# Kernel optimization log

Hardware: AMD Instinct MI355X
Metric: run time of the kernel (lower is better)

Reference implementation:

```python
import jax, jax.numpy as jnp
import numpy as np

V, H, B, S, J, T, NOP = 30000, 512, 16, 256, 10, 8, 4
NEG = -1e9


def setup_inputs() -> dict:
    key = jax.random.key(0)
    ks = jax.random.split(key, 10)
    return {
        "x": jax.random.randint(ks[0], (B, S), 0, V),
        "encoder_output": jax.random.normal(ks[1], (B, S, H), jnp.float32),
        "encoder_hidden": jax.random.normal(ks[2], (B, H), jnp.float32),
        "max_len": T,
        "emb_W": jax.random.normal(ks[3], (V, H), jnp.float32) * 0.02,
        "slot_emb": jax.random.normal(ks[4], (J, H), jnp.float32) * 0.1,
        "W_ih": jax.random.normal(ks[5], (3 * H, H), jnp.float32) * 0.02,
        "W_hh": jax.random.normal(ks[6], (3 * H, H), jnp.float32) * 0.02,
        "b_ih": jnp.zeros((3 * H,), jnp.float32),
        "b_hh": jnp.zeros((3 * H,), jnp.float32),
        "w_gen_W": jax.random.normal(ks[7], (1, 3 * H), jnp.float32) * 0.02,
        "w_gen_b": jnp.zeros((1,), jnp.float32),
        "action_W": jax.random.normal(ks[8], (NOP, H), jnp.float32) * 0.02,
        "action_b": jnp.zeros((NOP,), jnp.float32),
    }


def gru_step(xin, h, W_ih, W_hh, b_ih, b_hh):
    # xin, h: (J, B, H). PyTorch GRU gate order: r, z, n.
    gi = xin @ W_ih.T + b_ih
    gh = h @ W_hh.T + b_hh
    ir, iz, inn = jnp.split(gi, 3, axis=-1)
    hr, hz, hn = jnp.split(gh, 3, axis=-1)
    r = jax.nn.sigmoid(ir + hr)
    z = jax.nn.sigmoid(iz + hz)
    n = jnp.tanh(inn + r * hn)
    return (1.0 - z) * n + z * h


def reference(x, encoder_output, encoder_hidden, max_len, emb_W, slot_emb,
              W_ih, W_hh, b_ih, b_hh, w_gen_W, w_gen_b, action_W, action_b):
    nJ, nH = slot_emb.shape
    nB, nS = x.shape
    nV = emb_W.shape[0]
    mask = (x == 0)  # (B, S) pad mask
    xJ = jnp.broadcast_to(x[None], (nJ, nB, nS))
    jidx = jnp.arange(nJ)[:, None, None]
    bidx = jnp.arange(nB)[None, :, None]

    w0 = jnp.broadcast_to(slot_emb[:, None, :], (nJ, nB, nH))  # slot query per slot
    h0 = jnp.broadcast_to(encoder_hidden[None], (nJ, nB, nH))

    def step(carry, _):
        w, h = carry
        h = gru_step(w, h, W_ih, W_hh, b_ih, b_hh)
        # attention over encoder states
        attn_e = jnp.einsum('bsh,jbh->jbs', encoder_output, h)
        attn_e = jnp.where(mask[None], NEG, attn_e)
        attn_hist = jax.nn.softmax(attn_e, axis=-1)          # (J,B,S)
        context = jnp.einsum('jbs,bsh->jbh', attn_hist, encoder_output)
        # vocab distribution
        attn_vocab = jax.nn.softmax(h @ emb_W.T, axis=-1)    # (J,B,V)
        # pointer-generator mix
        gen_in = jnp.concatenate([w, h, context], axis=-1)   # (J,B,3H)
        p_gen = jax.nn.sigmoid(gen_in @ w_gen_W.T + w_gen_b) # (J,B,1)
        p_ctx = jnp.zeros((nJ, nB, nV), attn_vocab.dtype).at[jidx, bidx, xJ].add(attn_hist)
        p_final = p_gen * attn_vocab + (1.0 - p_gen) * p_ctx # (J,B,V)
        w_idx = jnp.argmax(p_final, axis=-1)                 # greedy next token
        w_next = emb_W[w_idx]                                # (J,B,H)
        return (w_next, h), (p_final, context)

    (_, _), (p_all, ctx_all) = jax.lax.scan(step, (w0, h0), None, length=max_len)
    # gate head uses context from first decode step (k == 0)
    gates = ctx_all[0] @ action_W.T + action_b               # (J,B,n_op)
    all_gate = jnp.transpose(gates, (1, 0, 2))               # (B,J,n_op)
    all_point = jnp.transpose(p_all, (2, 1, 0, 3))           # (B,J,T,V)
    return all_gate, all_point
```

## Files before the change

### kernel.cpp

```cpp
#include <hip/hip_runtime.h>
#include <math.h>

#define V 30000
#define H 512
#define NB 16
#define NS 256
#define NJ 10
#define NT 8
#define NOPS 4
#define NR 160
#define EV 30720
#define NEGV -1e9f

typedef __attribute__((ext_vector_type(8))) short short8;
typedef __attribute__((ext_vector_type(4))) short short4v;
typedef __attribute__((ext_vector_type(4))) float f32x4;

__device__ inline float bf2f(unsigned short s) {
    union { unsigned int u; float f; } c; c.u = ((unsigned int)s) << 16;
    return c.f;
}
__device__ inline unsigned short f2bf(float f) {
    union { float f; unsigned int u; } c; c.f = f;
    unsigned int u = c.u;
    u += 0x7fffu + ((u >> 16) & 1u);
    return (unsigned short)(u >> 16);
}
__device__ inline unsigned long long packkey(float f, int v) {
    union { float f; unsigned int u; } c; c.f = f;
    return ((unsigned long long)c.u << 32) | (unsigned int)(0x7FFFFFFF - v);
}

__global__ void k_setup_emb(const float* __restrict__ emb, unsigned short* __restrict__ emb_bf, int n8) {
    int gid = blockIdx.x * 256 + threadIdx.x;
    if (gid >= n8) return;
    const float4* src = (const float4*)emb + (size_t)gid * 2;
    float4 a = src[0], b = src[1];
    short8 o;
    o[0] = (short)f2bf(a.x); o[1] = (short)f2bf(a.y); o[2] = (short)f2bf(a.z); o[3] = (short)f2bf(a.w);
    o[4] = (short)f2bf(b.x); o[5] = (short)f2bf(b.y); o[6] = (short)f2bf(b.z); o[7] = (short)f2bf(b.w);
    *(short8*)(emb_bf + (size_t)gid * 8) = o;
}

__global__ void k_setup_small(const float* __restrict__ Wih, const float* __restrict__ Whh,
    unsigned short* wih_hi, unsigned short* wih_lo, unsigned short* whh_hi, unsigned short* whh_lo,
    const float* __restrict__ slot, const float* __restrict__ ench,
    float* w_g, unsigned short* w_hi, unsigned short* w_lo,
    float* h_g, unsigned short* h_hi, unsigned short* h_lo)
{
    int gid = blockIdx.x * 256 + threadIdx.x;
    if (gid < 786432) {
        float v1 = Wih[gid];
        unsigned short hi = f2bf(v1);
        wih_hi[gid] = hi; wih_lo[gid] = f2bf(v1 - bf2f(hi));
        float v2 = Whh[gid];
        hi = f2bf(v2);
        whh_hi[gid] = hi; whh_lo[gid] = f2bf(v2 - bf2f(hi));
    } else {
        int i = gid - 786432;
        if (i < NR * H) {
            int jb = i >> 9, d = i & 511;
            int j = jb >> 4, b = jb & 15;
            float wv = slot[j * H + d];
            w_g[i] = wv;
            unsigned short hi = f2bf(wv);
            w_hi[i] = hi; w_lo[i] = f2bf(wv - bf2f(hi));
            float hv = ench[b * H + d];
            h_g[i] = hv;
            hi = f2bf(hv);
            h_hi[i] = hi; h_lo[i] = f2bf(hv - bf2f(hi));
        }
    }
}

#define GRU_APAD 520
__global__ __launch_bounds__(256) void k_gru_gemm(
    const unsigned short* __restrict__ w_hi, const unsigned short* __restrict__ w_lo,
    const unsigned short* __restrict__ h_hi, const unsigned short* __restrict__ h_lo,
    const unsigned short* __restrict__ wih_hi, const unsigned short* __restrict__ wih_lo,
    const unsigned short* __restrict__ whh_hi, const unsigned short* __restrict__ whh_lo,
    float* __restrict__ gi, float* __restrict__ gh)
{
    __shared__ unsigned short Ah[16 * GRU_APAD];
    __shared__ unsigned short Al[16 * GRU_APAD];
    int nch = blockIdx.x, mt = blockIdx.y, z = blockIdx.z;
    const unsigned short* Asrc_hi = z ? h_hi : w_hi;
    const unsigned short* Asrc_lo = z ? h_lo : w_lo;
    const unsigned short* Bhi = z ? whh_hi : wih_hi;
    const unsigned short* Blo = z ? whh_lo : wih_lo;
    float* outp = z ? gh : gi;
    int t = threadIdx.x;
    for (int i = t; i < 2048; i += 256) {
        int matl = i >> 10;
        int row = (i >> 6) & 15;
        int seg = i & 63;
        const unsigned short* src = (matl ? Asrc_lo : Asrc_hi) + (mt * 16 + row) * 512 + seg * 8;
        unsigned short* dst = (matl ? Al : Ah) + row * GRU_APAD + seg * 8;
        *(short8*)dst = *(const short8*)src;
    }
    __syncthreads();
    int wv = t >> 6, lane = t & 63;
    int col15 = lane & 15, quad = lane >> 4;
    f32x4 acc0 = {0.f, 0.f, 0.f, 0.f}, acc1 = {0.f, 0.f, 0.f, 0.f};
    int c0 = nch * 128 + wv * 32 + col15;
    int c1 = c0 + 16;
    const unsigned short* bhp0 = Bhi + c0 * 512 + quad * 8;
    const unsigned short* bhp1 = Bhi + c1 * 512 + quad * 8;
    const unsigned short* blp0 = Blo + c0 * 512 + quad * 8;
    const unsigned short* blp1 = Blo + c1 * 512 + quad * 8;
    const unsigned short* ahp = Ah + col15 * GRU_APAD + quad * 8;
    const unsigned short* alp = Al + col15 * GRU_APAD + quad * 8;
#pragma unroll
    for (int ks = 0; ks < 16; ks++) {
        int ko = ks * 32;
        short8 bh0 = *(const short8*)(bhp0 + ko);
        short8 bh1 = *(const short8*)(bhp1 + ko);
        short8 bl0 = *(const short8*)(blp0 + ko);
        short8 bl1 = *(const short8*)(blp1 + ko);
        short8 ah = *(const short8*)(ahp + ko);
        short8 al = *(const short8*)(alp + ko);
        acc0 = __builtin_amdgcn_mfma_f32_16x16x32_bf16(ah, bh0, acc0, 0, 0, 0);
        acc1 = __builtin_amdgcn_mfma_f32_16x16x32_bf16(ah, bh1, acc1, 0, 0, 0);
        acc0 = __builtin_amdgcn_mfma_f32_16x16x32_bf16(ah, bl0, acc0, 0, 0, 0);
        acc1 = __builtin_amdgcn_mfma_f32_16x16x32_bf16(ah, bl1, acc1, 0, 0, 0);
        acc0 = __builtin_amdgcn_mfma_f32_16x16x32_bf16(al, bh0, acc0, 0, 0, 0);
        acc1 = __builtin_amdgcn_mfma_f32_16x16x32_bf16(al, bh1, acc1, 0, 0, 0);
    }
#pragma unroll
    for (int r = 0; r < 4; r++) {
        int row = mt * 16 + quad * 4 + r;
        outp[row * 1536 + c0] = acc0[r];
        outp[row * 1536 + c1] = acc1[r];
    }
}

__global__ __launch_bounds__(256) void k_attention(
    const float* __restrict__ gi, const float* __restrict__ gh,
    const float* __restrict__ b_ih, const float* __restrict__ b_hh,
    float* __restrict__ h_g, unsigned short* __restrict__ h_hi, unsigned short* __restrict__ h_lo,
    const float* __restrict__ enc, const int* __restrict__ x,
    const float* __restrict__ w_g, const float* __restrict__ wgenW, const float* __restrict__ wgenb,
    float* __restrict__ attn_g, float* __restrict__ pgen_g,
    float* __restrict__ ctx0, int store_ctx,
    float* __restrict__ rowsum, unsigned long long* __restrict__ argpk)
{
    __shared__ float h_lds[512];
    __shared__ float sc[256];
    __shared__ float red[256];
    __shared__ float ctxp[4 * 512];
    int jb = blockIdx.x;
    int b = jb & 15;
    int t = threadIdx.x;
    if (t == 0) { rowsum[jb] = 0.f; argpk[jb] = 0ull; }
    for (int d = t; d < 512; d += 256) {
        int base = jb * 1536;
        float ir = gi[base + d]        + b_ih[d];
        float iz = gi[base + 512 + d]  + b_ih[512 + d];
        float in = gi[base + 1024 + d] + b_ih[1024 + d];
        float hr = gh[base + d]        + b_hh[d];
        float hz = gh[base + 512 + d]  + b_hh[512 + d];
        float hn = gh[base + 1024 + d] + b_hh[1024 + d];
        float hold = h_g[jb * 512 + d];
        float r = 1.f / (1.f + expf(-(ir + hr)));
        float z = 1.f / (1.f + expf(-(iz + hz)));
        float n = tanhf(in + r * hn);
        float hnew = (1.f - z) * n + z * hold;
        h_lds[d] = hnew;
        h_g[jb * 512 + d] = hnew;
        unsigned short hi = f2bf(hnew);
        h_hi[jb * 512 + d] = hi;
        h_lo[jb * 512 + d] = f2bf(hnew - bf2f(hi));
    }
    __syncthreads();
    int wid = t >> 6, lane = t & 63;
    float hreg[8];
#pragma unroll
    for (int i = 0; i < 8; i++) hreg[i] = h_lds[lane * 8 + i];
    const float* encb = enc + (size_t)b * NS * H;
    for (int s = wid; s < NS; s += 4) {
        const float4* er = (const float4*)(encb + s * 512 + lane * 8);
        float4 e0 = er[0], e1 = er[1];
        float p = e0.x * hreg[0] + e0.y * hreg[1] + e0.z * hreg[2] + e0.w * hreg[3]
                + e1.x * hreg[4] + e1.y * hreg[5] + e1.z * hreg[6] + e1.w * hreg[7];
#pragma unroll
        for (int off = 32; off > 0; off >>= 1) p += __shfl_down(p, off);
        if (lane == 0) sc[s] = (x[b * NS + s] == 0) ? NEGV : p;
    }
    __syncthreads();
    red[t] = sc[t];
    __syncthreads();
    for (int sft = 128; sft > 0; sft >>= 1) { if (t < sft) red[t] = fmaxf(red[t], red[t + sft]); __syncthreads(); }
    float m = red[0];
    __syncthreads();
    float e = expf(sc[t] - m);
    red[t] = e;
    __syncthreads();
    for (int sft = 128; sft > 0; sft >>= 1) { if (t < sft) red[t] += red[t + sft]; __syncthreads(); }
    float inv = 1.f / red[0];
    float p_s = e * inv;
    sc[t] = p_s;
    attn_g[jb * NS + t] = p_s;
    __syncthreads();
    {
        float cp[8] = {0.f,0.f,0.f,0.f,0.f,0.f,0.f,0.f};
        const float* encw = encb + lane * 8;
        for (int s = wid * 64; s < wid * 64 + 64; s++) {
            float ps = sc[s];
            const float4* er = (const float4*)(encw + s * 512);
            float4 e0 = er[0], e1 = er[1];
            cp[0] += ps * e0.x; cp[1] += ps * e0.y; cp[2] += ps * e0.z; cp[3] += ps * e0.w;
            cp[4] += ps * e1.x; cp[5] += ps * e1.y; cp[6] += ps * e1.z; cp[7] += ps * e1.w;
        }
        float* cw = ctxp + wid * 512 + lane * 8;
#pragma unroll
        for (int i = 0; i < 8; i++) cw[i] = cp[i];
    }
    __syncthreads();
    int d0 = 2 * t, d1 = 2 * t + 1;
    float c0 = ctxp[d0] + ctxp[512 + d0] + ctxp[1024 + d0] + ctxp[1536 + d0];
    float c1 = ctxp[d1] + ctxp[512 + d1] + ctxp[1024 + d1] + ctxp[1536 + d1];
    if (store_ctx) ((float2*)ctx0)[jb * 256 + t] = make_float2(c0, c1);
    float pg = wgenW[d0] * w_g[jb * 512 + d0] + wgenW[d1] * w_g[jb * 512 + d1]
             + wgenW[512 + d0] * h_lds[d0] + wgenW[512 + d1] * h_lds[d1]
             + wgenW[1024 + d0] * c0 + wgenW[1024 + d1] * c1;
    __syncthreads();
    red[t] = pg;
    __syncthreads();
    for (int sft = 128; sft > 0; sft >>= 1) { if (t < sft) red[t] += red[t + sft]; __syncthreads(); }
    if (t == 0) pgen_g[jb] = 1.f / (1.f + expf(-(red[0] + wgenb[0])));
}

#define VPAD 136
__global__ __launch_bounds__(256) void k_vgemm(
    const unsigned short* __restrict__ h_hi, const unsigned short* __restrict__ emb_bf,
    unsigned short* __restrict__ E, float* __restrict__ rowsum,
    unsigned long long* __restrict__ argpk)
{
    __shared__ unsigned short A[160 * VPAD];
    int blk = blockIdx.x;
    int t = threadIdx.x;
    int wv = t >> 6, lane = t & 63, col15 = lane & 15, quad = lane >> 4;
    int v = blk * 128 + wv * 32 + col15;
    f32x4 acc[10][2];
#pragma unroll
    for (int m = 0; m < 10; m++) {
        acc[m][0] = (f32x4){0.f, 0.f, 0.f, 0.f};
        acc[m][1] = (f32x4){0.f, 0.f, 0.f, 0.f};
    }
    int v0c = min(v, V - 1);
    int v1c = min(v + 16, V - 1);
    for (int kc = 0; kc < 4; kc++) {
        __syncthreads();
        for (int i = t; i < 2560; i += 256) {
            int row = i >> 4, seg = i & 15;
            *(short8*)(A + row * VPAD + seg * 8) = *(const short8*)(h_hi + row * 512 + kc * 128 + seg * 8);
        }
        __syncthreads();
#pragma unroll
        for (int ks = 0; ks < 4; ks++) {
            int kl = ks * 32 + quad * 8;
            int kg = kc * 128 + kl;
            short8 b0 = *(const short8*)(emb_bf + (size_t)v0c * 512 + kg);
            short8 b1 = *(const short8*)(emb_bf + (size_t)v1c * 512 + kg);
#pragma unroll
            for (int m = 0; m < 10; m++) {
                short8 a = *(const short8*)(A + (m * 16 + col15) * VPAD + kl);
                acc[m][0] = __builtin_amdgcn_mfma_f32_16x16x32_bf16(a, b0, acc[m][0], 0, 0, 0);
                acc[m][1] = __builtin_amdgcn_mfma_f32_16x16x32_bf16(a, b1, acc[m][1], 0, 0, 0);
            }
        }
    }
    __syncthreads();
#pragma unroll
    for (int m = 0; m < 10; m++) {
#pragma unroll
        for (int tile = 0; tile < 2; tile++) {
            int vv = v + tile * 16;
            int cl = wv * 32 + tile * 16 + col15;
#pragma unroll
            for (int r = 0; r < 4; r++) {
                int row = m * 16 + quad * 4 + r;
                float ev = (vv < V) ? expf(acc[m][tile][r]) : 0.f;
                A[row * VPAD + cl] = f2bf(ev);
            }
        }
    }
    __syncthreads();
    if (t < 160) {
        float s = 0.f;
        unsigned long long key = 0ull;
#pragma unroll
        for (int seg = 0; seg < 16; seg++) {
            short8 ev = *(const short8*)(A + t * VPAD + seg * 8);
#pragma unroll
            for (int k = 0; k < 8; k++) {
                float f = bf2f((unsigned short)ev[k]);
                s += f;
                unsigned long long kk = packkey(f, blk * 128 + seg * 8 + k);
                key = (kk > key) ? kk : key;
            }
        }
        atomicAdd(rowsum + t, s);
        atomicMax(argpk + t, key);
    }
    {
        int rsub = t >> 4, seg = t & 15;
        for (int it = 0; it < 10; it++) {
            int row = it * 16 + rsub;
            short8 ev = *(const short8*)(A + row * VPAD + seg * 8);
            *(short8*)(E + (size_t)row * EV + blk * 128 + seg * 8) = ev;
        }
    }
}

__global__ __launch_bounds__(256) void k_finalize(
    const unsigned short* __restrict__ E, const float* __restrict__ pgen_g,
    const float* __restrict__ rowsum, const unsigned long long* __restrict__ argpk,
    const float* __restrict__ attn_g, const int* __restrict__ x,
    const float* __restrict__ emb, float* __restrict__ out,
    float* __restrict__ w_g, unsigned short* __restrict__ w_hi, unsigned short* __restrict__ w_lo,
    const float* __restrict__ ctx0, const float* __restrict__ aW, const float* __restrict__ ab,
    int tstep)
{
    __shared__ float bvs[256];
    __shared__ int bis[256];
    __shared__ float red[256];
    int jb = blockIdx.x, t = threadIdx.x;
    int j = jb >> 4, b = jb & 15;
    float inv = 1.f / rowsum[jb];
    float pgen = pgen_g[jb];
    float scale = pgen * inv;
    const unsigned short* Er = E + (size_t)jb * EV;
    size_t outbase = (size_t)640 + ((size_t)(b * NJ + j) * NT + tstep) * V;
    float* op = out + outbase;
    for (int c = 0; c < 29; c++) {
        int vv = c * 1024 + t * 4;
        short4v e = *(const short4v*)(Er + vv);
        float4 p = make_float4(bf2f((unsigned short)e[0]) * scale, bf2f((unsigned short)e[1]) * scale,
                               bf2f((unsigned short)e[2]) * scale, bf2f((unsigned short)e[3]) * scale);
        *(float4*)(op + vv) = p;
    }
    if (t < 76) {
        int vv = 29696 + t * 4;
        short4v e = *(const short4v*)(Er + vv);
        float4 p = make_float4(bf2f((unsigned short)e[0]) * scale, bf2f((unsigned short)e[1]) * scale,
                               bf2f((unsigned short)e[2]) * scale, bf2f((unsigned short)e[3]) * scale);
        *(float4*)(op + vv) = p;
    }
    __syncthreads();
    float best; int besti;
    {
        int vv = x[b * NS + t];
        float a = (1.f - pgen) * attn_g[jb * NS + t];
        float old = atomicAdd(&op[vv], a);
        best = old + a;
        besti = vv;
    }
    bvs[t] = best; bis[t] = besti;
    __syncthreads();
    for (int sft = 128; sft > 0; sft >>= 1) {
        if (t < sft) {
            if (bvs[t + sft] > bvs[t] || (bvs[t + sft] == bvs[t] && bis[t + sft] < bis[t])) {
                bvs[t] = bvs[t + sft]; bis[t] = bis[t + sft];
            }
        }
        __syncthreads();
    }
    int widx;
    {
        unsigned long long key = argpk[jb];
        union { unsigned int u; float f; } c; c.u = (unsigned int)(key >> 32);
        float db = c.f * scale;
        int di = 0x7FFFFFFF - (int)(key & 0xFFFFFFFFu);
        float sb = bvs[0]; int si = bis[0];
        widx = (sb > db || (sb == db && si < di)) ? si : di;
    }
    for (int d = t; d < 512; d += 256) {
        float val = emb[(size_t)widx * 512 + d];
        w_g[jb * 512 + d] = val;
        unsigned short hi = f2bf(val);
        w_hi[jb * 512 + d] = hi;
        w_lo[jb * 512 + d] = f2bf(val - bf2f(hi));
    }
    if (tstep == 0) {
        float part[4] = {0.f, 0.f, 0.f, 0.f};
        for (int d = t; d < 512; d += 256) {
            float c = ctx0[jb * 512 + d];
#pragma unroll
            for (int o = 0; o < 4; o++) part[o] += c * aW[o * 512 + d];
        }
        for (int o = 0; o < 4; o++) {
            __syncthreads();
            red[t] = part[o];
            __syncthreads();
            for (int sft = 128; sft > 0; sft >>= 1) { if (t < sft) red[t] += red[t + sft]; __syncthreads(); }
            if (t == 0) out[(b * NJ + j) * NOPS + o] = red[0] + ab[o];
        }
    }
}

extern "C" void kernel_launch(void* const* d_in, const int* in_sizes, int n_in,
                              void* d_out, int out_size, void* d_ws, size_t ws_size,
                              hipStream_t stream) {
    const int*   x     = (const int*)d_in[0];
    const float* enc   = (const float*)d_in[1];
    const float* ench  = (const float*)d_in[2];
    const float* embW  = (const float*)d_in[4];
    const float* slot  = (const float*)d_in[5];
    const float* Wih   = (const float*)d_in[6];
    const float* Whh   = (const float*)d_in[7];
    const float* bih   = (const float*)d_in[8];
    const float* bhh   = (const float*)d_in[9];
    const float* wgenW = (const float*)d_in[10];
    const float* wgenb = (const float*)d_in[11];
    const float* aW    = (const float*)d_in[12];
    const float* ab    = (const float*)d_in[13];
    float* out = (float*)d_out;

    char* ws = (char*)d_ws;
    size_t off = 0;
    auto carve = [&](size_t bytes) { char* p = ws + off; off += (bytes + 255) & ~(size_t)255; return p; };
    unsigned short* emb_bf = (unsigned short*)carve((size_t)V * H * 2);
    unsigned short* wih_hi = (unsigned short*)carve(786432 * 2);
    unsigned short* wih_lo = (unsigned short*)carve(786432 * 2);
    unsigned short* whh_hi = (unsigned short*)carve(786432 * 2);
    unsigned short* whh_lo = (unsigned short*)carve(786432 * 2);
    float* w_f32 = (float*)carve(NR * H * 4);
    float* h_f32 = (float*)carve(NR * H * 4);
    float* ctx0  = (float*)carve(NR * H * 4);
    unsigned short* w_hi = (unsigned short*)carve(NR * H * 2);
    unsigned short* w_lo = (unsigned short*)carve(NR * H * 2);
    unsigned short* h_hi = (unsigned short*)carve(NR * H * 2);
    unsigned short* h_lo = (unsigned short*)carve(NR * H * 2);
    float* gi   = (float*)carve(NR * 1536 * 4);
    float* gh   = (float*)carve(NR * 1536 * 4);
    float* attn = (float*)carve(NR * NS * 4);
    float* pgen = (float*)carve(NR * 4);
    float* rowsum = (float*)carve(NR * 4);
    unsigned long long* argpk = (unsigned long long*)carve(NR * 8);
    unsigned short* E = (unsigned short*)carve((size_t)NR * EV * 2);

    k_setup_emb<<<7500, 256, 0, stream>>>(embW, emb_bf, (V * H) / 8);
    k_setup_small<<<3392, 256, 0, stream>>>(Wih, Whh, wih_hi, wih_lo, whh_hi, whh_lo,
                                            slot, ench, w_f32, w_hi, w_lo, h_f32, h_hi, h_lo);
    for (int t = 0; t < NT; t++) {
        k_gru_gemm<<<dim3(12, 10, 2), 256, 0, stream>>>(w_hi, w_lo, h_hi, h_lo,
                                                        wih_hi, wih_lo, whh_hi, whh_lo, gi, gh);
        k_attention<<<NR, 256, 0, stream>>>(gi, gh, bih, bhh, h_f32, h_hi, h_lo, enc, x,
                                            w_f32, wgenW, wgenb, attn, pgen, ctx0, t == 0 ? 1 : 0,
                                            rowsum, argpk);
        k_vgemm<<<240, 256, 0, stream>>>(h_hi, emb_bf, E, rowsum, argpk);
        k_finalize<<<NR, 256, 0, stream>>>(E, pgen, rowsum, argpk, attn, x, embW, out,
                                           w_f32, w_hi, w_lo, ctx0, aW, ab, t);
    }
}
```

Before: 1.100 ms.

## Fuse attention with vocab GEMM via spin-wait flag and overlap hidden GEMM with finalize

```diff
diff --git a/kernel.cpp b/kernel.cpp
--- a/kernel.cpp
+++ b/kernel.cpp
@@ -46,9 +46,11 @@
     unsigned short* wih_hi, unsigned short* wih_lo, unsigned short* whh_hi, unsigned short* whh_lo,
     const float* __restrict__ slot, const float* __restrict__ ench,
     float* w_g, unsigned short* w_hi, unsigned short* w_lo,
-    float* h_g, unsigned short* h_hi, unsigned short* h_lo)
+    float* h_g, unsigned short* h_hi, unsigned short* h_lo,
+    unsigned int* hcnt)
 {
     int gid = blockIdx.x * 256 + threadIdx.x;
+    if (gid == 0) *hcnt = 0u;
     if (gid < 786432) {
         float v1 = Wih[gid];
         unsigned short hi = f2bf(v1);
@@ -74,21 +76,13 @@
 }
 
 #define GRU_APAD 520
-__global__ __launch_bounds__(256) void k_gru_gemm(
-    const unsigned short* __restrict__ w_hi, const unsigned short* __restrict__ w_lo,
-    const unsigned short* __restrict__ h_hi, const unsigned short* __restrict__ h_lo,
-    const unsigned short* __restrict__ wih_hi, const unsigned short* __restrict__ wih_lo,
-    const unsigned short* __restrict__ whh_hi, const unsigned short* __restrict__ whh_lo,
-    float* __restrict__ gi, float* __restrict__ gh)
+__device__ __forceinline__ void gru_gemm_body(
+    int nch, int mt,
+    const unsigned short* __restrict__ Asrc_hi, const unsigned short* __restrict__ Asrc_lo,
+    const unsigned short* __restrict__ Bhi, const unsigned short* __restrict__ Blo,
+    float* __restrict__ outp,
+    unsigned short* Ah, unsigned short* Al)
 {
-    __shared__ unsigned short Ah[16 * GRU_APAD];
-    __shared__ unsigned short Al[16 * GRU_APAD];
-    int nch = blockIdx.x, mt = blockIdx.y, z = blockIdx.z;
-    const unsigned short* Asrc_hi = z ? h_hi : w_hi;
-    const unsigned short* Asrc_lo = z ? h_lo : w_lo;
-    const unsigned short* Bhi = z ? whh_hi : wih_hi;
-    const unsigned short* Blo = z ? whh_lo : wih_lo;
-    float* outp = z ? gh : gi;
     int t = threadIdx.x;
     for (int i = t; i < 2048; i += 256) {
         int matl = i >> 10;
@@ -134,7 +128,22 @@
     }
 }
 
-__global__ __launch_bounds__(256) void k_attention(
+__global__ __launch_bounds__(256) void k_gi(
+    const unsigned short* __restrict__ w_hi, const unsigned short* __restrict__ w_lo,
+    const unsigned short* __restrict__ wih_hi, const unsigned short* __restrict__ wih_lo,
+    float* __restrict__ gi)
+{
+    __shared__ unsigned short Ah[16 * GRU_APAD];
+    __shared__ unsigned short Al[16 * GRU_APAD];
+    int nch = blockIdx.x % 12, mt = blockIdx.x / 12;
+    gru_gemm_body(nch, mt, w_hi, w_lo, wih_hi, wih_lo, gi, Ah, Al);
+}
+
+#define VPAD 136
+struct AttnSmem { float h_lds[512]; float sc[256]; float red[256]; float ctxp[4 * 512]; };
+union CSmem { unsigned short A[160 * VPAD]; AttnSmem at; };
+
+__global__ __launch_bounds__(256, 2) void k_attn_vgemm(
     const float* __restrict__ gi, const float* __restrict__ gh,
     const float* __restrict__ b_ih, const float* __restrict__ b_hh,
     float* __restrict__ h_g, unsigned short* __restrict__ h_hi, unsigned short* __restrict__ h_lo,
@@ -142,189 +151,205 @@
     const float* __restrict__ w_g, const float* __restrict__ wgenW, const float* __restrict__ wgenb,
     float* __restrict__ attn_g, float* __restrict__ pgen_g,
     float* __restrict__ ctx0, int store_ctx,
-    float* __restrict__ rowsum, unsigned long long* __restrict__ argpk)
+    float* __restrict__ rowsum, unsigned long long* __restrict__ argpk,
+    const unsigned short* __restrict__ emb_bf, unsigned short* __restrict__ E,
+    unsigned int* hcnt, unsigned int htarget)
 {
-    __shared__ float h_lds[512];
-    __shared__ float sc[256];
-    __shared__ float red[256];
-    __shared__ float ctxp[4 * 512];
-    int jb = blockIdx.x;
-    int b = jb & 15;
-    int t = threadIdx.x;
-    if (t == 0) { rowsum[jb] = 0.f; argpk[jb] = 0ull; }
-    for (int d = t; d < 512; d += 256) {
-        int base = jb * 1536;
-        float ir = gi[base + d]        + b_ih[d];
-        float iz = gi[base + 512 + d]  + b_ih[512 + d];
-        float in = gi[base + 1024 + d] + b_ih[1024 + d];
-        float hr = gh[base + d]        + b_hh[d];
-        float hz = gh[base + 512 + d]  + b_hh[512 + d];
-        float hn = gh[base + 1024 + d] + b_hh[1024 + d];
-        float hold = h_g[jb * 512 + d];
-        float r = 1.f / (1.f + expf(-(ir + hr)));
-        float z = 1.f / (1.f + expf(-(iz + hz)));
-        float n = tanhf(in + r * hn);
-        float hnew = (1.f - z) * n + z * hold;
-        h_lds[d] = hnew;
-        h_g[jb * 512 + d] = hnew;
-        unsigned short hi = f2bf(hnew);
-        h_hi[jb * 512 + d] = hi;
-        h_lo[jb * 512 + d] = f2bf(hnew - bf2f(hi));
-    }
-    __syncthreads();
-    int wid = t >> 6, lane = t & 63;
-    float hreg[8];
-#pragma unroll
-    for (int i = 0; i < 8; i++) hreg[i] = h_lds[lane * 8 + i];
-    const float* encb = enc + (size_t)b * NS * H;
-    for (int s = wid; s < NS; s += 4) {
-        const float4* er = (const float4*)(encb + s * 512 + lane * 8);
-        float4 e0 = er[0], e1 = er[1];
-        float p = e0.x * hreg[0] + e0.y * hreg[1] + e0.z * hreg[2] + e0.w * hreg[3]
-                + e1.x * hreg[4] + e1.y * hreg[5] + e1.z * hreg[6] + e1.w * hreg[7];
-#pragma unroll
-        for (int off = 32; off > 0; off >>= 1) p += __shfl_down(p, off);
-        if (lane == 0) sc[s] = (x[b * NS + s] == 0) ? NEGV : p;
-    }
-    __syncthreads();
-    red[t] = sc[t];
-    __syncthreads();
-    for (int sft = 128; sft > 0; sft >>= 1) { if (t < sft) red[t] = fmaxf(red[t], red[t + sft]); __syncthreads(); }
-    float m = red[0];
-    __syncthreads();
-    float e = expf(sc[t] - m);
-    red[t] = e;
-    __syncthreads();
-    for (int sft = 128; sft > 0; sft >>= 1) { if (t < sft) red[t] += red[t + sft]; __syncthreads(); }
-    float inv = 1.f / red[0];
-    float p_s = e * inv;
-    sc[t] = p_s;
-    attn_g[jb * NS + t] = p_s;
-    __syncthreads();
-    {
-        float cp[8] = {0.f,0.f,0.f,0.f,0.f,0.f,0.f,0.f};
-        const float* encw = encb + lane * 8;
-        for (int s = wid * 64; s < wid * 64 + 64; s++) {
-            float ps = sc[s];
-            const float4* er = (const float4*)(encw + s * 512);
+    __shared__ CSmem sm;
+    if (blockIdx.x < 160) {
+        float* h_lds = sm.at.h_lds;
+        float* sc    = sm.at.sc;
+        float* red   = sm.at.red;
+        float* ctxp  = sm.at.ctxp;
+        int jb = blockIdx.x;
+        int b = jb & 15;
+        int t = threadIdx.x;
+        if (t == 0) { rowsum[jb] = 0.f; argpk[jb] = 0ull; }
+        for (int d = t; d < 512; d += 256) {
+            int base = jb * 1536;
+            float ir = gi[base + d]        + b_ih[d];
+            float iz = gi[base + 512 + d]  + b_ih[512 + d];
+            float in = gi[base + 1024 + d] + b_ih[1024 + d];
+            float hr = gh[base + d]        + b_hh[d];
+            float hz = gh[base + 512 + d]  + b_hh[512 + d];
+            float hn = gh[base + 1024 + d] + b_hh[1024 + d];
+            float hold = h_g[jb * 512 + d];
+            float r = 1.f / (1.f + expf(-(ir + hr)));
+            float z = 1.f / (1.f + expf(-(iz + hz)));
+            float n = tanhf(in + r * hn);
+            float hnew = (1.f - z) * n + z * hold;
+            h_lds[d] = hnew;
+            h_g[jb * 512 + d] = hnew;
+            unsigned short hi = f2bf(hnew);
+            h_hi[jb * 512 + d] = hi;
+            h_lo[jb * 512 + d] = f2bf(hnew - bf2f(hi));
+        }
+        __syncthreads();
+        if (t == 0) { __threadfence(); atomicAdd(hcnt, 1u); }
+        int wid = t >> 6, lane = t & 63;
+        float hreg[8];
+#pragma unroll
+        for (int i = 0; i < 8; i++) hreg[i] = h_lds[lane * 8 + i];
+        const float* encb = enc + (size_t)b * NS * H;
+        for (int s = wid; s < NS; s += 4) {
+            const float4* er = (const float4*)(encb + s * 512 + lane * 8);
             float4 e0 = er[0], e1 = er[1];
-            cp[0] += ps * e0.x; cp[1] += ps * e0.y; cp[2] += ps * e0.z; cp[3] += ps * e0.w;
-            cp[4] += ps * e1.x; cp[5] += ps * e1.y; cp[6] += ps * e1.z; cp[7] += ps * e1.w;
-        }
-        float* cw = ctxp + wid * 512 + lane * 8;
-#pragma unroll
-        for (int i = 0; i < 8; i++) cw[i] = cp[i];
-    }
-    __syncthreads();
-    int d0 = 2 * t, d1 = 2 * t + 1;
-    float c0 = ctxp[d0] + ctxp[512 + d0] + ctxp[1024 + d0] + ctxp[1536 + d0];
-    float c1 = ctxp[d1] + ctxp[512 + d1] + ctxp[1024 + d1] + ctxp[1536 + d1];
-    if (store_ctx) ((float2*)ctx0)[jb * 256 + t] = make_float2(c0, c1);
-    float pg = wgenW[d0] * w_g[jb * 512 + d0] + wgenW[d1] * w_g[jb * 512 + d1]
-             + wgenW[512 + d0] * h_lds[d0] + wgenW[512 + d1] * h_lds[d1]
-             + wgenW[1024 + d0] * c0 + wgenW[1024 + d1] * c1;
-    __syncthreads();
-    red[t] = pg;
-    __syncthreads();
-    for (int sft = 128; sft > 0; sft >>= 1) { if (t < sft) red[t] += red[t + sft]; __syncthreads(); }
-    if (t == 0) pgen_g[jb] = 1.f / (1.f + expf(-(red[0] + wgenb[0])));
-}
-
-#define VPAD 136
-__global__ __launch_bounds__(256) void k_vgemm(
-    const unsigned short* __restrict__ h_hi, const unsigned short* __restrict__ emb_bf,
-    unsigned short* __restrict__ E, float* __restrict__ rowsum,
-    unsigned long long* __restrict__ argpk)
-{
-    __shared__ unsigned short A[160 * VPAD];
-    int blk = blockIdx.x;
-    int t = threadIdx.x;
-    int wv = t >> 6, lane = t & 63, col15 = lane & 15, quad = lane >> 4;
-    int v = blk * 128 + wv * 32 + col15;
-    f32x4 acc[10][2];
-#pragma unroll
-    for (int m = 0; m < 10; m++) {
-        acc[m][0] = (f32x4){0.f, 0.f, 0.f, 0.f};
-        acc[m][1] = (f32x4){0.f, 0.f, 0.f, 0.f};
-    }
-    int v0c = min(v, V - 1);
-    int v1c = min(v + 16, V - 1);
-    for (int kc = 0; kc < 4; kc++) {
-        __syncthreads();
-        for (int i = t; i < 2560; i += 256) {
-            int row = i >> 4, seg = i & 15;
-            *(short8*)(A + row * VPAD + seg * 8) = *(const short8*)(h_hi + row * 512 + kc * 128 + seg * 8);
-        }
-        __syncthreads();
-#pragma unroll
-        for (int ks = 0; ks < 4; ks++) {
-            int kl = ks * 32 + quad * 8;
-            int kg = kc * 128 + kl;
-            short8 b0 = *(const short8*)(emb_bf + (size_t)v0c * 512 + kg);
-            short8 b1 = *(const short8*)(emb_bf + (size_t)v1c * 512 + kg);
-#pragma unroll
-            for (int m = 0; m < 10; m++) {
-                short8 a = *(const short8*)(A + (m * 16 + col15) * VPAD + kl);
-                acc[m][0] = __builtin_amdgcn_mfma_f32_16x16x32_bf16(a, b0, acc[m][0], 0, 0, 0);
-                acc[m][1] = __builtin_amdgcn_mfma_f32_16x16x32_bf16(a, b1, acc[m][1], 0, 0, 0);
-            }
-        }
-    }
-    __syncthreads();
-#pragma unroll
-    for (int m = 0; m < 10; m++) {
-#pragma unroll
-        for (int tile = 0; tile < 2; tile++) {
-            int vv = v + tile * 16;
-            int cl = wv * 32 + tile * 16 + col15;
-#pragma unroll
-            for (int r = 0; r < 4; r++) {
-                int row = m * 16 + quad * 4 + r;
-                float ev = (vv < V) ? expf(acc[m][tile][r]) : 0.f;
-                A[row * VPAD + cl] = f2bf(ev);
-            }
-        }
-    }
-    __syncthreads();
-    if (t < 160) {
-        float s = 0.f;
-        unsigned long long key = 0ull;
-#pragma unroll
-        for (int seg = 0; seg < 16; seg++) {
-            short8 ev = *(const short8*)(A + t * VPAD + seg * 8);
-#pragma unroll
-            for (int k = 0; k < 8; k++) {
-                float f = bf2f((unsigned short)ev[k]);
-                s += f;
-                unsigned long long kk = packkey(f, blk * 128 + seg * 8 + k);
-                key = (kk > key) ? kk : key;
-            }
-        }
-        atomicAdd(rowsum + t, s);
-        atomicMax(argpk + t, key);
-    }
-    {
-        int rsub = t >> 4, seg = t & 15;
-        for (int it = 0; it < 10; it++) {
-            int row = it * 16 + rsub;
-            short8 ev = *(const short8*)(A + row * VPAD + seg * 8);
-            *(short8*)(E + (size_t)row * EV + blk * 128 + seg * 8) = ev;
-        }
-    }
-}
-
-__global__ __launch_bounds__(256) void k_finalize(
+            float p = e0.x * hreg[0] + e0.y * hreg[1] + e0.z * hreg[2] + e0.w * hreg[3]
+                    + e1.x * hreg[4] + e1.y * hreg[5] + e1.z * hreg[6] + e1.w * hreg[7];
+#pragma unroll
+            for (int off = 32; off > 0; off >>= 1) p += __shfl_down(p, off);
+            if (lane == 0) sc[s] = (x[b * NS + s] == 0) ? NEGV : p;
+        }
+        __syncthreads();
+        red[t] = sc[t];
+        __syncthreads();
+        for (int sft = 128; sft > 0; sft >>= 1) { if (t < sft) red[t] = fmaxf(red[t], red[t + sft]); __syncthreads(); }
+        float m = red[0];
+        __syncthreads();
+        float e = expf(sc[t] - m);
+        red[t] = e;
+        __syncthreads();
+        for (int sft = 128; sft > 0; sft >>= 1) { if (t < sft) red[t] += red[t + sft]; __syncthreads(); }
+        float inv = 1.f / red[0];
+        float p_s = e * inv;
+        sc[t] = p_s;
+        attn_g[jb * NS + t] = p_s;
+        __syncthreads();
+        {
+            float cp[8] = {0.f,0.f,0.f,0.f,0.f,0.f,0.f,0.f};
+            const float* encw = encb + lane * 8;
+            for (int s = wid * 64; s < wid * 64 + 64; s++) {
+                float ps = sc[s];
+                const float4* er = (const float4*)(encw + s * 512);
+                float4 e0 = er[0], e1 = er[1];
+                cp[0] += ps * e0.x; cp[1] += ps * e0.y; cp[2] += ps * e0.z; cp[3] += ps * e0.w;
+                cp[4] += ps * e1.x; cp[5] += ps * e1.y; cp[6] += ps * e1.z; cp[7] += ps * e1.w;
+            }
+            float* cw = ctxp + wid * 512 + lane * 8;
+#pragma unroll
+            for (int i = 0; i < 8; i++) cw[i] = cp[i];
+        }
+        __syncthreads();
+        int d0 = 2 * t, d1 = 2 * t + 1;
+        float c0 = ctxp[d0] + ctxp[512 + d0] + ctxp[1024 + d0] + ctxp[1536 + d0];
+        float c1 = ctxp[d1] + ctxp[512 + d1] + ctxp[1024 + d1] + ctxp[1536 + d1];
+        if (store_ctx) ((float2*)ctx0)[jb * 256 + t] = make_float2(c0, c1);
+        float pg = wgenW[d0] * w_g[jb * 512 + d0] + wgenW[d1] * w_g[jb * 512 + d1]
+                 + wgenW[512 + d0] * h_lds[d0] + wgenW[512 + d1] * h_lds[d1]
+                 + wgenW[1024 + d0] * c0 + wgenW[1024 + d1] * c1;
+        __syncthreads();
+        red[t] = pg;
+        __syncthreads();
+        for (int sft = 128; sft > 0; sft >>= 1) { if (t < sft) red[t] += red[t + sft]; __syncthreads(); }
+        if (t == 0) pgen_g[jb] = 1.f / (1.f + expf(-(red[0] + wgenb[0])));
+    } else {
+        unsigned short* A = sm.A;
+        int blk = blockIdx.x - 160;
+        int t = threadIdx.x;
+        if (t == 0) {
+            while (__hip_atomic_load(hcnt, __ATOMIC_ACQUIRE, __HIP_MEMORY_SCOPE_AGENT) < htarget)
+                __builtin_amdgcn_s_sleep(2);
+            __threadfence();
+        }
+        __syncthreads();
+        int wv = t >> 6, lane = t & 63, col15 = lane & 15, quad = lane >> 4;
+        int v = blk * 128 + wv * 32 + col15;
+        f32x4 acc[10][2];
+#pragma unroll
+        for (int m = 0; m < 10; m++) {
+            acc[m][0] = (f32x4){0.f, 0.f, 0.f, 0.f};
+            acc[m][1] = (f32x4){0.f, 0.f, 0.f, 0.f};
+        }
+        int v0c = min(v, V - 1);
+        int v1c = min(v + 16, V - 1);
+        for (int kc = 0; kc < 4; kc++) {
+            __syncthreads();
+            for (int i = t; i < 2560; i += 256) {
+                int row = i >> 4, seg = i & 15;
+                *(short8*)(A + row * VPAD + seg * 8) = *(const short8*)(h_hi + row * 512 + kc * 128 + seg * 8);
+            }
+            __syncthreads();
+#pragma unroll
+            for (int ks = 0; ks < 4; ks++) {
+                int kl = ks * 32 + quad * 8;
+                int kg = kc * 128 + kl;
+                short8 b0 = *(const short8*)(emb_bf + (size_t)v0c * 512 + kg);
+                short8 b1 = *(const short8*)(emb_bf + (size_t)v1c * 512 + kg);
+#pragma unroll
+                for (int m = 0; m < 10; m++) {
+                    short8 a = *(const short8*)(A + (m * 16 + col15) * VPAD + kl);
+                    acc[m][0] = __builtin_amdgcn_mfma_f32_16x16x32_bf16(a, b0, acc[m][0], 0, 0, 0);
+                    acc[m][1] = __builtin_amdgcn_mfma_f32_16x16x32_bf16(a, b1, acc[m][1], 0, 0, 0);
+                }
+            }
+        }
+        __syncthreads();
+#pragma unroll
+        for (int m = 0; m < 10; m++) {
+#pragma unroll
+            for (int tile = 0; tile < 2; tile++) {
+                int vv = v + tile * 16;
+                int cl = wv * 32 + tile * 16 + col15;
+#pragma unroll
+                for (int r = 0; r < 4; r++) {
+                    int row = m * 16 + quad * 4 + r;
+                    float ev = (vv < V) ? expf(acc[m][tile][r]) : 0.f;
+                    A[row * VPAD + cl] = f2bf(ev);
+                }
+            }
+        }
+        __syncthreads();
+        if (t < 160) {
+            float s = 0.f;
+            unsigned long long key = 0ull;
+#pragma unroll
+            for (int seg = 0; seg < 16; seg++) {
+                short8 ev = *(const short8*)(A + t * VPAD + seg * 8);
+#pragma unroll
+                for (int k = 0; k < 8; k++) {
+                    float f = bf2f((unsigned short)ev[k]);
+                    s += f;
+                    unsigned long long kk = packkey(f, blk * 128 + seg * 8 + k);
+                    key = (kk > key) ? kk : key;
+                }
+            }
+            atomicAdd(rowsum + t, s);
+            atomicMax(argpk + t, key);
+        }
+        {
+            int rsub = t >> 4, seg = t & 15;
+            for (int it = 0; it < 10; it++) {
+                int row = it * 16 + rsub;
+                short8 ev = *(const short8*)(A + row * VPAD + seg * 8);
+                *(short8*)(E + (size_t)row * EV + blk * 128 + seg * 8) = ev;
+            }
+        }
+    }
+}
+
+__global__ __launch_bounds__(256) void k_fin_gh(
     const unsigned short* __restrict__ E, const float* __restrict__ pgen_g,
     const float* __restrict__ rowsum, const unsigned long long* __restrict__ argpk,
     const float* __restrict__ attn_g, const int* __restrict__ x,
     const float* __restrict__ emb, float* __restrict__ out,
     float* __restrict__ w_g, unsigned short* __restrict__ w_hi, unsigned short* __restrict__ w_lo,
     const float* __restrict__ ctx0, const float* __restrict__ aW, const float* __restrict__ ab,
-    int tstep)
+    int tstep, int nfin,
+    const unsigned short* __restrict__ h_hi, const unsigned short* __restrict__ h_lo,
+    const unsigned short* __restrict__ whh_hi, const unsigned short* __restrict__ whh_lo,
+    float* __restrict__ gh)
 {
     __shared__ float bvs[256];
     __shared__ int bis[256];
     __shared__ float red[256];
+    if ((int)blockIdx.x >= nfin) {
+        __shared__ unsigned short Ah[16 * GRU_APAD];
+        __shared__ unsigned short Al[16 * GRU_APAD];
+        int idx = blockIdx.x - nfin;
+        int nch = idx % 12, mt = idx / 12;
+        gru_gemm_body(nch, mt, h_hi, h_lo, whh_hi, whh_lo, gh, Ah, Al);
+        return;
+    }
     int jb = blockIdx.x, t = threadIdx.x;
     int j = jb >> 4, b = jb & 15;
     float inv = 1.f / rowsum[jb];
@@ -333,19 +358,25 @@
     const unsigned short* Er = E + (size_t)jb * EV;
     size_t outbase = (size_t)640 + ((size_t)(b * NJ + j) * NT + tstep) * V;
     float* op = out + outbase;
-    for (int c = 0; c < 29; c++) {
-        int vv = c * 1024 + t * 4;
-        short4v e = *(const short4v*)(Er + vv);
-        float4 p = make_float4(bf2f((unsigned short)e[0]) * scale, bf2f((unsigned short)e[1]) * scale,
-                               bf2f((unsigned short)e[2]) * scale, bf2f((unsigned short)e[3]) * scale);
-        *(float4*)(op + vv) = p;
-    }
-    if (t < 76) {
-        int vv = 29696 + t * 4;
-        short4v e = *(const short4v*)(Er + vv);
-        float4 p = make_float4(bf2f((unsigned short)e[0]) * scale, bf2f((unsigned short)e[1]) * scale,
-                               bf2f((unsigned short)e[2]) * scale, bf2f((unsigned short)e[3]) * scale);
-        *(float4*)(op + vv) = p;
+    for (int c = 0; c < 14; c++) {
+        int vv = c * 2048 + t * 8;
+        short8 e = *(const short8*)(Er + vv);
+        float4 p0 = make_float4(bf2f((unsigned short)e[0]) * scale, bf2f((unsigned short)e[1]) * scale,
+                                bf2f((unsigned short)e[2]) * scale, bf2f((unsigned short)e[3]) * scale);
+        float4 p1 = make_float4(bf2f((unsigned short)e[4]) * scale, bf2f((unsigned short)e[5]) * scale,
+                                bf2f((unsigned short)e[6]) * scale, bf2f((unsigned short)e[7]) * scale);
+        *(float4*)(op + vv) = p0;
+        *(float4*)(op + vv + 4) = p1;
+    }
+    if (t < 166) {
+        int vv = 28672 + t * 8;
+        short8 e = *(const short8*)(Er + vv);
+        float4 p0 = make_float4(bf2f((unsigned short)e[0]) * scale, bf2f((unsigned short)e[1]) * scale,
+                                bf2f((unsigned short)e[2]) * scale, bf2f((unsigned short)e[3]) * scale);
+        float4 p1 = make_float4(bf2f((unsigned short)e[4]) * scale, bf2f((unsigned short)e[5]) * scale,
+                                bf2f((unsigned short)e[6]) * scale, bf2f((unsigned short)e[7]) * scale);
+        *(float4*)(op + vv) = p0;
+        *(float4*)(op + vv + 4) = p1;
     }
     __syncthreads();
     float best; int besti;
@@ -438,19 +469,24 @@
     float* pgen = (float*)carve(NR * 4);
     float* rowsum = (float*)carve(NR * 4);
     unsigned long long* argpk = (unsigned long long*)carve(NR * 8);
+    unsigned int* hcnt = (unsigned int*)carve(4);
     unsigned short* E = (unsigned short*)carve((size_t)NR * EV * 2);
 
     k_setup_emb<<<7500, 256, 0, stream>>>(embW, emb_bf, (V * H) / 8);
     k_setup_small<<<3392, 256, 0, stream>>>(Wih, Whh, wih_hi, wih_lo, whh_hi, whh_lo,
-                                            slot, ench, w_f32, w_hi, w_lo, h_f32, h_hi, h_lo);
+                                            slot, ench, w_f32, w_hi, w_lo, h_f32, h_hi, h_lo, hcnt);
+    k_fin_gh<<<120, 256, 0, stream>>>(E, pgen, rowsum, argpk, attn, x, embW, out,
+                                      w_f32, w_hi, w_lo, ctx0, aW, ab, 0, 0,
+                                      h_hi, h_lo, whh_hi, whh_lo, gh);
     for (int t = 0; t < NT; t++) {
-        k_gru_gemm<<<dim3(12, 10, 2), 256, 0, stream>>>(w_hi, w_lo, h_hi, h_lo,
-                                                        wih_hi, wih_lo, whh_hi, whh_lo, gi, gh);
-        k_attention<<<NR, 256, 0, stream>>>(gi, gh, bih, bhh, h_f32, h_hi, h_lo, enc, x,
-                                            w_f32, wgenW, wgenb, attn, pgen, ctx0, t == 0 ? 1 : 0,
-                                            rowsum, argpk);
-        k_vgemm<<<240, 256, 0, stream>>>(h_hi, emb_bf, E, rowsum, argpk);
-        k_finalize<<<NR, 256, 0, stream>>>(E, pgen, rowsum, argpk, attn, x, embW, out,
-                                           w_f32, w_hi, w_lo, ctx0, aW, ab, t);
-    }
-}
+        k_gi<<<120, 256, 0, stream>>>(w_hi, w_lo, wih_hi, wih_lo, gi);
+        k_attn_vgemm<<<400, 256, 0, stream>>>(gi, gh, bih, bhh, h_f32, h_hi, h_lo, enc, x,
+                                              w_f32, wgenW, wgenb, attn, pgen, ctx0, t == 0 ? 1 : 0,
+                                              rowsum, argpk, emb_bf, E,
+                                              hcnt, (unsigned)(t + 1) * 160u);
+        int nblk = (t < NT - 1) ? 280 : 160;
+        k_fin_gh<<<nblk, 256, 0, stream>>>(E, pgen, rowsum, argpk, attn, x, embW, out,
+                                           w_f32, w_hi, w_lo, ctx0, aW, ab, t, 160,
+                                           h_hi, h_lo, whh_hi, whh_lo, gh);
+    }
+}
```

Result: slower. 1.177 ms (+6.9%).

## Halve vocab GEMM block width, read hidden rows from global, widen finalize loads

Applied to the files above, without the earlier changes.

```diff
diff --git a/kernel.cpp b/kernel.cpp
--- a/kernel.cpp
+++ b/kernel.cpp
@@ -230,59 +230,40 @@
     if (t == 0) pgen_g[jb] = 1.f / (1.f + expf(-(red[0] + wgenb[0])));
 }
 
-#define VPAD 136
+#define VBLK 64
+#define LDSP 76
 __global__ __launch_bounds__(256) void k_vgemm(
     const unsigned short* __restrict__ h_hi, const unsigned short* __restrict__ emb_bf,
     unsigned short* __restrict__ E, float* __restrict__ rowsum,
     unsigned long long* __restrict__ argpk)
 {
-    __shared__ unsigned short A[160 * VPAD];
+    __shared__ unsigned short A[160 * LDSP];
     int blk = blockIdx.x;
     int t = threadIdx.x;
     int wv = t >> 6, lane = t & 63, col15 = lane & 15, quad = lane >> 4;
-    int v = blk * 128 + wv * 32 + col15;
-    f32x4 acc[10][2];
+    int v = blk * VBLK + wv * 16 + col15;
+    int vc = min(v, V - 1);
+    f32x4 acc[10];
+#pragma unroll
+    for (int m = 0; m < 10; m++) acc[m] = (f32x4){0.f, 0.f, 0.f, 0.f};
+    const unsigned short* bp = emb_bf + (size_t)vc * 512 + quad * 8;
+    const unsigned short* ap = h_hi + col15 * 512 + quad * 8;
+#pragma unroll 4
+    for (int ks = 0; ks < 16; ks++) {
+        short8 b = *(const short8*)(bp + ks * 32);
+#pragma unroll
+        for (int m = 0; m < 10; m++) {
+            short8 a = *(const short8*)(ap + m * 8192 + ks * 32);
+            acc[m] = __builtin_amdgcn_mfma_f32_16x16x32_bf16(a, b, acc[m], 0, 0, 0);
+        }
+    }
 #pragma unroll
     for (int m = 0; m < 10; m++) {
-        acc[m][0] = (f32x4){0.f, 0.f, 0.f, 0.f};
-        acc[m][1] = (f32x4){0.f, 0.f, 0.f, 0.f};
-    }
-    int v0c = min(v, V - 1);
-    int v1c = min(v + 16, V - 1);
-    for (int kc = 0; kc < 4; kc++) {
-        __syncthreads();
-        for (int i = t; i < 2560; i += 256) {
-            int row = i >> 4, seg = i & 15;
-            *(short8*)(A + row * VPAD + seg * 8) = *(const short8*)(h_hi + row * 512 + kc * 128 + seg * 8);
-        }
-        __syncthreads();
-#pragma unroll
-        for (int ks = 0; ks < 4; ks++) {
-            int kl = ks * 32 + quad * 8;
-            int kg = kc * 128 + kl;
-            short8 b0 = *(const short8*)(emb_bf + (size_t)v0c * 512 + kg);
-            short8 b1 = *(const short8*)(emb_bf + (size_t)v1c * 512 + kg);
-#pragma unroll
-            for (int m = 0; m < 10; m++) {
-                short8 a = *(const short8*)(A + (m * 16 + col15) * VPAD + kl);
-                acc[m][0] = __builtin_amdgcn_mfma_f32_16x16x32_bf16(a, b0, acc[m][0], 0, 0, 0);
-                acc[m][1] = __builtin_amdgcn_mfma_f32_16x16x32_bf16(a, b1, acc[m][1], 0, 0, 0);
-            }
-        }
-    }
-    __syncthreads();
-#pragma unroll
-    for (int m = 0; m < 10; m++) {
-#pragma unroll
-        for (int tile = 0; tile < 2; tile++) {
-            int vv = v + tile * 16;
-            int cl = wv * 32 + tile * 16 + col15;
-#pragma unroll
-            for (int r = 0; r < 4; r++) {
-                int row = m * 16 + quad * 4 + r;
-                float ev = (vv < V) ? expf(acc[m][tile][r]) : 0.f;
-                A[row * VPAD + cl] = f2bf(ev);
-            }
+#pragma unroll
+        for (int r = 0; r < 4; r++) {
+            int row = m * 16 + quad * 4 + r;
+            float ev = (v < V) ? expf(acc[m][r]) : 0.f;
+            A[row * LDSP + wv * 16 + col15] = f2bf(ev);
         }
     }
     __syncthreads();
@@ -290,13 +271,13 @@
         float s = 0.f;
         unsigned long long key = 0ull;
 #pragma unroll
-        for (int seg = 0; seg < 16; seg++) {
-            short8 ev = *(const short8*)(A + t * VPAD + seg * 8);
+        for (int seg = 0; seg < 8; seg++) {
+            short8 ev = *(const short8*)(A + t * LDSP + seg * 8);
 #pragma unroll
             for (int k = 0; k < 8; k++) {
                 float f = bf2f((unsigned short)ev[k]);
                 s += f;
-                unsigned long long kk = packkey(f, blk * 128 + seg * 8 + k);
+                unsigned long long kk = packkey(f, blk * VBLK + seg * 8 + k);
                 key = (kk > key) ? kk : key;
             }
         }
@@ -304,11 +285,11 @@
         atomicMax(argpk + t, key);
     }
     {
-        int rsub = t >> 4, seg = t & 15;
-        for (int it = 0; it < 10; it++) {
-            int row = it * 16 + rsub;
-            short8 ev = *(const short8*)(A + row * VPAD + seg * 8);
-            *(short8*)(E + (size_t)row * EV + blk * 128 + seg * 8) = ev;
+        int rsub = t >> 3, seg = t & 7;
+        for (int it = 0; it < 5; it++) {
+            int row = it * 32 + rsub;
+            short8 ev = *(const short8*)(A + row * LDSP + seg * 8);
+            *(short8*)(E + (size_t)row * EV + blk * VBLK + seg * 8) = ev;
         }
     }
 }
@@ -333,19 +314,25 @@
     const unsigned short* Er = E + (size_t)jb * EV;
     size_t outbase = (size_t)640 + ((size_t)(b * NJ + j) * NT + tstep) * V;
     float* op = out + outbase;
-    for (int c = 0; c < 29; c++) {
-        int vv = c * 1024 + t * 4;
-        short4v e = *(const short4v*)(Er + vv);
-        float4 p = make_float4(bf2f((unsigned short)e[0]) * scale, bf2f((unsigned short)e[1]) * scale,
-                               bf2f((unsigned short)e[2]) * scale, bf2f((unsigned short)e[3]) * scale);
-        *(float4*)(op + vv) = p;
-    }
-    if (t < 76) {
-        int vv = 29696 + t * 4;
-        short4v e = *(const short4v*)(Er + vv);
-        float4 p = make_float4(bf2f((unsigned short)e[0]) * scale, bf2f((unsigned short)e[1]) * scale,
-                               bf2f((unsigned short)e[2]) * scale, bf2f((unsigned short)e[3]) * scale);
-        *(float4*)(op + vv) = p;
+    for (int c = 0; c < 14; c++) {
+        int vv = c * 2048 + t * 8;
+        short8 e = *(const short8*)(Er + vv);
+        float4 p0 = make_float4(bf2f((unsigned short)e[0]) * scale, bf2f((unsigned short)e[1]) * scale,
+                                bf2f((unsigned short)e[2]) * scale, bf2f((unsigned short)e[3]) * scale);
+        float4 p1 = make_float4(bf2f((unsigned short)e[4]) * scale, bf2f((unsigned short)e[5]) * scale,
+                                bf2f((unsigned short)e[6]) * scale, bf2f((unsigned short)e[7]) * scale);
+        *(float4*)(op + vv) = p0;
+        *(float4*)(op + vv + 4) = p1;
+    }
+    if (t < 166) {
+        int vv = 28672 + t * 8;
+        short8 e = *(const short8*)(Er + vv);
+        float4 p0 = make_float4(bf2f((unsigned short)e[0]) * scale, bf2f((unsigned short)e[1]) * scale,
+                                bf2f((unsigned short)e[2]) * scale, bf2f((unsigned short)e[3]) * scale);
+        float4 p1 = make_float4(bf2f((unsigned short)e[4]) * scale, bf2f((unsigned short)e[5]) * scale,
+                                bf2f((unsigned short)e[6]) * scale, bf2f((unsigned short)e[7]) * scale);
+        *(float4*)(op + vv) = p0;
+        *(float4*)(op + vv + 4) = p1;
     }
     __syncthreads();
     float best; int besti;
@@ -449,7 +436,7 @@
         k_attention<<<NR, 256, 0, stream>>>(gi, gh, bih, bhh, h_f32, h_hi, h_lo, enc, x,
                                             w_f32, wgenW, wgenb, attn, pgen, ctx0, t == 0 ? 1 : 0,
                                             rowsum, argpk);
-        k_vgemm<<<240, 256, 0, stream>>>(h_hi, emb_bf, E, rowsum, argpk);
+        k_vgemm<<<469, 256, 0, stream>>>(h_hi, emb_bf, E, rowsum, argpk);
         k_finalize<<<NR, 256, 0, stream>>>(E, pgen, rowsum, argpk, attn, x, embW, out,
                                            w_f32, w_hi, w_lo, ctx0, aW, ab, t);
     }
```

Result: slower. 1.262 ms (+14.7%).
